# Kernel tuning notes

Hardware: AMD Instinct MI355X
Metric: run time of the kernel (lower is better)

Reference implementation:

```python
import jax, jax.numpy as jnp
import numpy as np

B = 16384
S = 7
CELL = 1.0 / 7.0   # CELL_SILE
LC = 5.0           # lambda_coord
LN = 0.5           # lambda_noobj


def setup_inputs() -> dict:
    key = jax.random.key(0)
    k1, k2, k3 = jax.random.split(key, 3)
    predictions = jax.random.normal(k1, (B, S, S, 30), dtype=jnp.float32)
    targets = jax.random.uniform(k2, (B, S, S, 30), dtype=jnp.float32)
    # channel 4 is the objectness flag; code requires it to be exactly 0 or 1
    conf = (jax.random.uniform(k3, (B, S, S)) < 0.25).astype(jnp.float32)
    targets = targets.at[..., 4].set(conf)
    return {"predictions": predictions, "targets": targets}


def _box_corners(xy, wh):
    # Faithful to the original in-place bug: x2y2 uses the ALREADY-UPDATED x1y1
    xy1 = xy * CELL - wh * 0.5
    xy2 = xy1 * CELL + wh * 0.5
    return xy1, xy2


def _loss_terms(predictions, targets):
    p = predictions.reshape(-1, 30)   # [N, 30], N = B*S*S
    t = targets.reshape(-1, 30)
    obj = (t[:, 4] == 1.0).astype(p.dtype)
    noobj = (t[:, 4] == 0.0).astype(p.dtype)

    # no-object confidence loss on cols 4 and 9
    noobj_loss = LN * jnp.sum(noobj * (jnp.square(p[:, 4] - t[:, 4]) + jnp.square(p[:, 9] - t[:, 9])))

    # two predicted boxes per cell: cols 0:4 and 5:9 ; wh are sqrt-encoded -> square
    pb = jnp.stack([p[:, 0:4], p[:, 5:9]], axis=1)        # [N, 2, 4]
    pxy1, pxy2 = _box_corners(pb[..., 0:2], jnp.square(pb[..., 2:4]))  # [N,2,2]
    txy1, txy2 = _box_corners(t[:, None, 0:2], jnp.square(t[:, None, 2:4]))  # [N,1,2]

    # torchvision.ops.box_iou math (no clamp on areas, clamp(0) on intersection)
    lt = jnp.maximum(pxy1, txy1)
    rb = jnp.minimum(pxy2, txy2)
    inter = jnp.prod(jnp.clip(rb - lt, 0.0, None), axis=-1)   # [N, 2]
    area_p = jnp.prod(pxy2 - pxy1, axis=-1)                   # [N, 2]
    area_t = jnp.prod(txy2 - txy1, axis=-1)                   # [N, 1]
    iou = inter / (area_p + area_t - inter)                   # [N, 2]

    idx = jnp.argmax(iou, axis=1)                             # responsible box in {0,1}

    cols = idx[:, None] * 5 + jnp.arange(4)[None, :]          # [N, 4]
    cp = jnp.take_along_axis(p, cols, axis=1)
    ct = jnp.take_along_axis(t, cols, axis=1)
    center_loss = LC * jnp.sum(obj * jnp.sum(jnp.square(cp[:, 0:2] - ct[:, 0:2]), axis=1))
    wh_loss = LC * jnp.sum(obj * jnp.sum(jnp.square(cp[:, 2:4] - ct[:, 2:4]), axis=1))

    ccol = (idx * 5 + 4)[:, None]
    conf_loss = LC * jnp.sum(obj * jnp.square(jnp.take_along_axis(p, ccol, axis=1) - jnp.take_along_axis(t, ccol, axis=1))[:, 0])

    kcol = (jnp.argmax(t[:, 10:30], axis=1) + 10)[:, None]
    cls_loss = LC * jnp.sum(obj * jnp.square(jnp.take_along_axis(p, kcol, axis=1) - jnp.take_along_axis(t, kcol, axis=1))[:, 0])

    total = noobj_loss + center_loss + wh_loss + conf_loss + cls_loss
    return cls_loss, conf_loss, center_loss + wh_loss, total


def reference(predictions, targets):
    return _loss_terms(predictions, targets)
```

## Files before the change

### kernel.cpp

```cpp
#include <hip/hip_runtime.h>


constexpr int   BLK   = 128;
constexpr int   TILE  = 128;
constexpr int   NC    = 16384 * 7 * 7;
constexpr int   NTILE = NC / TILE;
constexpr int   GRID  = 3136;
constexpr float CELL  = 1.0f / 7.0f;
constexpr float LC    = 5.0f;
constexpr float LN    = 0.5f;

__device__ inline void gload_lds16(const float4* g, float4* l)
{
    __builtin_amdgcn_global_load_lds(
        (const __attribute__((address_space(1))) void*)g,
        (__attribute__((address_space(3))) void*)l,
        16, 0, 0);
}

__launch_bounds__(BLK, 3)
__global__ void yolo_partial(const float* __restrict__ P, const float* __restrict__ T,
                             float4* __restrict__ ws)
{
    __shared__ float4 s4[1920];
    __shared__ float red[4][2];

    const int tid = threadIdx.x;
    float a_cls = 0.f, a_conf = 0.f, a_cw = 0.f, a_noobj = 0.f;

    for (int t = blockIdx.x; t < NTILE; t += GRID) {
        const size_t fbase = (size_t)t * (TILE * 30);
        const float4* gT = reinterpret_cast<const float4*>(T + fbase);
        const float4* gP = reinterpret_cast<const float4*>(P + fbase);

        #pragma unroll
        for (int k = 0; k < 15; ++k) {
            const int idx = k * BLK + tid;
            const float4* g = (idx < 960) ? (gT + idx) : (gP + (idx - 960));
            gload_lds16(g, s4 + idx);
        }
        __syncthreads();

        const float* sf  = reinterpret_cast<const float*>(s4);
        const float* myT = sf + (size_t)tid * 30;
        const float* myP = sf + 3840 + (size_t)tid * 30;
        float tv[30], pv[30];
        #pragma unroll
        for (int j = 0; j < 15; ++j) {
            float2 a = reinterpret_cast<const float2*>(myT)[j];
            tv[2 * j] = a.x; tv[2 * j + 1] = a.y;
            float2 b = reinterpret_cast<const float2*>(myP)[j];
            pv[2 * j] = b.x; pv[2 * j + 1] = b.y;
        }

        float best = tv[10], pk = pv[10];
        #pragma unroll
        for (int k = 11; k < 30; ++k) {
            if (tv[k] > best) { best = tv[k]; pk = pv[k]; }
        }

        const float t4    = tv[4];
        const float obj   = (t4 == 1.0f) ? 1.0f : 0.0f;
        const float noobj = (t4 == 0.0f) ? 1.0f : 0.0f;

        float d4 = pv[4] - t4;
        float d9 = pv[9] - tv[9];
        a_noobj += noobj * (d4 * d4 + d9 * d9);

        float tw2 = tv[2] * tv[2], th2 = tv[3] * tv[3];
        float tx1 = tv[0] * CELL - 0.5f * tw2;
        float tx2 = tx1 * CELL + 0.5f * tw2;
        float ty1 = tv[1] * CELL - 0.5f * th2;
        float ty2 = ty1 * CELL + 0.5f * th2;
        float area_t = (tx2 - tx1) * (ty2 - ty1);

        float iou0, iou1;
        #pragma unroll
        for (int b = 0; b < 2; ++b) {
            float bw2 = pv[5 * b + 2] * pv[5 * b + 2];
            float bh2 = pv[5 * b + 3] * pv[5 * b + 3];
            float px1 = pv[5 * b + 0] * CELL - 0.5f * bw2;
            float px2 = px1 * CELL + 0.5f * bw2;
            float py1 = pv[5 * b + 1] * CELL - 0.5f * bh2;
            float py2 = py1 * CELL + 0.5f * bh2;
            float ltx = fmaxf(px1, tx1), lty = fmaxf(py1, ty1);
            float rbx = fminf(px2, tx2), rby = fminf(py2, ty2);
            float inter = fmaxf(rbx - ltx, 0.0f) * fmaxf(rby - lty, 0.0f);
            float area_p = (px2 - px1) * (py2 - py1);
            float iou = inter / (area_p + area_t - inter);
            if (b == 0) iou0 = iou; else iou1 = iou;
        }
        const bool b1 = (iou1 > iou0);

        float cpx = b1 ? pv[5] : pv[0], ctx = b1 ? tv[5] : tv[0];
        float cpy = b1 ? pv[6] : pv[1], cty = b1 ? tv[6] : tv[1];
        float cpw = b1 ? pv[7] : pv[2], ctw = b1 ? tv[7] : tv[2];
        float cph = b1 ? pv[8] : pv[3], cth = b1 ? tv[8] : tv[3];
        float cpc = b1 ? pv[9] : pv[4], ctc = b1 ? tv[9] : tv[4];

        float dx = cpx - ctx, dy = cpy - cty;
        float dw = cpw - ctw, dh = cph - cth;
        a_cw   += obj * (dx * dx + dy * dy + dw * dw + dh * dh);
        float dc = cpc - ctc;
        a_conf += obj * dc * dc;
        float dk = pk - best;
        a_cls  += obj * dk * dk;

        __syncthreads();
    }

    float vals[4] = { a_cls, a_conf, a_cw, a_noobj };
    #pragma unroll
    for (int c = 0; c < 4; ++c) {
        #pragma unroll
        for (int off = 32; off > 0; off >>= 1)
            vals[c] += __shfl_down(vals[c], off, 64);
    }
    const int wave = tid >> 6;
    if ((tid & 63) == 0) {
        red[0][wave] = vals[0]; red[1][wave] = vals[1];
        red[2][wave] = vals[2]; red[3][wave] = vals[3];
    }
    __syncthreads();
    if (tid == 0) {
        ws[blockIdx.x] = make_float4(red[0][0] + red[0][1],
                                     red[1][0] + red[1][1],
                                     red[2][0] + red[2][1],
                                     red[3][0] + red[3][1]);
    }
}

__launch_bounds__(1024, 1)
__global__ void yolo_reduce(const float4* __restrict__ ws, float* __restrict__ out)
{
    __shared__ float red[4][16];
    const int tid = threadIdx.x;

    float s0 = 0.f, s1 = 0.f, s2 = 0.f, s3 = 0.f;
    for (int b = tid; b < GRID; b += 1024) {
        float4 v = ws[b];
        s0 += v.x; s1 += v.y; s2 += v.z; s3 += v.w;
    }
    float vals[4] = { s0, s1, s2, s3 };
    #pragma unroll
    for (int c = 0; c < 4; ++c) {
        #pragma unroll
        for (int off = 32; off > 0; off >>= 1)
            vals[c] += __shfl_down(vals[c], off, 64);
        if ((tid & 63) == 0) red[c][tid >> 6] = vals[c];
    }
    __syncthreads();
    if (tid == 0) {
        float t0 = 0.f, t1 = 0.f, t2 = 0.f, t3 = 0.f;
        #pragma unroll
        for (int w = 0; w < 16; ++w) {
            t0 += red[0][w]; t1 += red[1][w]; t2 += red[2][w]; t3 += red[3][w];
        }
        out[0] = LC * t0;
        out[1] = LC * t1;
        out[2] = LC * t2;
        out[3] = LN * t3 + LC * (t0 + t1 + t2);
    }
}

extern "C" void kernel_launch(void* const* d_in, const int* in_sizes, int n_in,
                              void* d_out, int out_size, void* d_ws, size_t ws_size,
                              hipStream_t stream) {
    const float* P = (const float*)d_in[0];
    const float* T = (const float*)d_in[1];
    float* out = (float*)d_out;
    float4* ws = (float4*)d_ws;

    yolo_partial<<<GRID, BLK, 0, stream>>>(P, T, ws);
    yolo_reduce<<<1, 1024, 0, stream>>>(ws, out);
}
```

Measured before the change: 205.5 us.

## Use single-wave blocks with double-buffered LDS prefetch and no barriers

```diff
diff --git a/kernel.cpp b/kernel.cpp
--- a/kernel.cpp
+++ b/kernel.cpp
@@ -1,11 +1,12 @@
 #include <hip/hip_runtime.h>
 
 
-constexpr int   BLK   = 128;
-constexpr int   TILE  = 128;
+constexpr int   BLK   = 64;
+constexpr int   TILE  = 64;
 constexpr int   NC    = 16384 * 7 * 7;
 constexpr int   NTILE = NC / TILE;
 constexpr int   GRID  = 3136;
+constexpr int   ITERS = NTILE / GRID;
 constexpr float CELL  = 1.0f / 7.0f;
 constexpr float LC    = 5.0f;
 constexpr float LN    = 0.5f;
@@ -18,32 +19,44 @@
         16, 0, 0);
 }
 
-__launch_bounds__(BLK, 3)
+__device__ inline void stage_tile(const float* __restrict__ P,
+                                  const float* __restrict__ T,
+                                  int t, float4* dst, int lane)
+{
+    const float4* gT = reinterpret_cast<const float4*>(T + (size_t)t * 1920);
+    const float4* gP = reinterpret_cast<const float4*>(P + (size_t)t * 1920);
+    #pragma unroll
+    for (int k = 0; k < 15; ++k) {
+        const int idx = k * 64 + lane;
+        gload_lds16(idx < 480 ? gT + idx : gP + (idx - 480), dst + idx);
+    }
+}
+
+__launch_bounds__(BLK, 4)
 __global__ void yolo_partial(const float* __restrict__ P, const float* __restrict__ T,
                              float4* __restrict__ ws)
 {
     __shared__ float4 s4[1920];
-    __shared__ float red[4][2];
+    const int lane = threadIdx.x;
 
-    const int tid = threadIdx.x;
     float a_cls = 0.f, a_conf = 0.f, a_cw = 0.f, a_noobj = 0.f;
 
-    for (int t = blockIdx.x; t < NTILE; t += GRID) {
-        const size_t fbase = (size_t)t * (TILE * 30);
-        const float4* gT = reinterpret_cast<const float4*>(T + fbase);
-        const float4* gP = reinterpret_cast<const float4*>(P + fbase);
+    stage_tile(P, T, blockIdx.x, s4, lane);
 
-        #pragma unroll
-        for (int k = 0; k < 15; ++k) {
-            const int idx = k * BLK + tid;
-            const float4* g = (idx < 960) ? (gT + idx) : (gP + (idx - 960));
-            gload_lds16(g, s4 + idx);
-        }
-        __syncthreads();
+    #pragma unroll
+    for (int it = 0; it < ITERS; ++it) {
+        const int cur = it & 1;
 
-        const float* sf  = reinterpret_cast<const float*>(s4);
-        const float* myT = sf + (size_t)tid * 30;
-        const float* myP = sf + 3840 + (size_t)tid * 30;
+        if (it + 1 < ITERS)
+            stage_tile(P, T, blockIdx.x + (it + 1) * GRID, s4 + ((it + 1) & 1) * 960, lane);
+
+        if (it + 1 < ITERS) asm volatile("s_waitcnt vmcnt(15)" ::: "memory");
+        else                asm volatile("s_waitcnt vmcnt(0)"  ::: "memory");
+        __builtin_amdgcn_sched_barrier(0);
+
+        const float* sf  = reinterpret_cast<const float*>(s4 + cur * 960);
+        const float* myT = sf + (size_t)lane * 30;
+        const float* myP = sf + 1920 + (size_t)lane * 30;
         float tv[30], pv[30];
         #pragma unroll
         for (int j = 0; j < 15; ++j) {
@@ -106,7 +119,8 @@
         float dk = pk - best;
         a_cls  += obj * dk * dk;
 
-        __syncthreads();
+        asm volatile("s_waitcnt lgkmcnt(0)" ::: "memory");
+        __builtin_amdgcn_sched_barrier(0);
     }
 
     float vals[4] = { a_cls, a_conf, a_cw, a_noobj };
@@ -116,18 +130,8 @@
         for (int off = 32; off > 0; off >>= 1)
             vals[c] += __shfl_down(vals[c], off, 64);
     }
-    const int wave = tid >> 6;
-    if ((tid & 63) == 0) {
-        red[0][wave] = vals[0]; red[1][wave] = vals[1];
-        red[2][wave] = vals[2]; red[3][wave] = vals[3];
-    }
-    __syncthreads();
-    if (tid == 0) {
-        ws[blockIdx.x] = make_float4(red[0][0] + red[0][1],
-                                     red[1][0] + red[1][1],
-                                     red[2][0] + red[2][1],
-                                     red[3][0] + red[3][1]);
-    }
+    if (lane == 0)
+        ws[blockIdx.x] = make_float4(vals[0], vals[1], vals[2], vals[3]);
 }
 
 __launch_bounds__(1024, 1)
```

Measured after the change: 208.9 us. About the same (+1.7%).
